# Kernel optimization log

Hardware: AMD Instinct MI355X
Metric: run time of the kernel (lower is better)

The kernel has to match this reference:

```python
import jax, jax.numpy as jnp
import numpy as np

N, E, IN, H, OUT = 50000, 600000, 256, 128, 40
EPS, GAMMA = 0.1, 0.1  # PyG AntiSymmetricConv defaults


def _build_norm(edge_index, n):
    # GCNConv normalization with added self loops: D^-1/2 (A+I) D^-1/2
    loops = jnp.arange(n, dtype=edge_index.dtype)
    src = jnp.concatenate([edge_index[0], loops])
    dst = jnp.concatenate([edge_index[1], loops])
    deg = jax.ops.segment_sum(jnp.ones(src.shape[0], dtype=jnp.float32), dst, num_segments=n)
    dinv = jnp.where(deg > 0, jax.lax.rsqrt(jnp.maximum(deg, 1e-12)), 0.0)
    return src, dst, dinv[src] * dinv[dst]


def _gcn(x, w, src, dst, norm, n):
    # GCNConv(bias=False): scatter normalized messages to target nodes
    m = (x @ w)[src] * norm[:, None]          # [E+N, d]
    return jax.ops.segment_sum(m, dst, num_segments=n)


def _antisym_conv(x, W, gcn_w, bias, src, dst, norm, num_iters):
    d = W.shape[0]
    aW = W - W.T - GAMMA * jnp.eye(d, dtype=W.dtype)  # antisymmetric weight
    n = x.shape[0]

    def step(h, _):
        upd = jnp.tanh(h @ aW.T + _gcn(h, gcn_w, src, dst, norm, n) + bias)
        return h + EPS * upd, None

    x, _ = jax.lax.scan(step, x, None, length=num_iters)
    return x


def setup_inputs() -> dict:
    key = jax.random.key(0)
    ks = jax.random.split(key, 16)
    s = lambda fan: 1.0 / np.sqrt(fan)
    return {
        "x": jax.random.normal(ks[0], (N, IN), dtype=jnp.float32),
        "edge_index": jax.random.randint(ks[1], (2, E), 0, N, dtype=jnp.int64),
        "w_hid": jax.random.normal(ks[2], (H, IN), dtype=jnp.float32) * s(IN),
        "b_hid": jax.random.normal(ks[3], (H,), dtype=jnp.float32) * s(IN),
        "W_a1": jax.random.normal(ks[4], (H, H), dtype=jnp.float32) * s(H),
        "gcn_w1": jax.random.normal(ks[5], (H, H), dtype=jnp.float32) * s(H),
        "b_a1": jax.random.normal(ks[6], (H,), dtype=jnp.float32) * s(H),
        "w_hid2": jax.random.normal(ks[7], (H // 2, H), dtype=jnp.float32) * s(H),
        "b_hid2": jax.random.normal(ks[8], (H // 2,), dtype=jnp.float32) * s(H),
        "W_a2": jax.random.normal(ks[9], (H // 2, H // 2), dtype=jnp.float32) * s(H // 2),
        "gcn_w2": jax.random.normal(ks[10], (H // 2, H // 2), dtype=jnp.float32) * s(H // 2),
        "b_a2": jax.random.normal(ks[11], (H // 2,), dtype=jnp.float32) * s(H // 2),
        "w_fc": jax.random.normal(ks[12], (OUT, H // 2), dtype=jnp.float32) * s(H // 2),
        "b_fc": jax.random.normal(ks[13], (OUT,), dtype=jnp.float32) * s(H // 2),
    }


def reference(x, edge_index, w_hid, b_hid, W_a1, gcn_w1, b_a1,
              w_hid2, b_hid2, W_a2, gcn_w2, b_a2, w_fc, b_fc):
    n = x.shape[0]
    src, dst, norm = _build_norm(edge_index, n)
    h = jax.nn.leaky_relu(x @ w_hid.T + b_hid)          # dropout is no-op in eval
    h = _antisym_conv(h, W_a1, gcn_w1, b_a1, src, dst, norm, num_iters=3)
    h = jax.nn.leaky_relu(h)
    h = jax.nn.leaky_relu(h @ w_hid2.T + b_hid2)
    h = _antisym_conv(h, W_a2, gcn_w2, b_a2, src, dst, norm, num_iters=1)
    out = h @ w_fc.T + b_fc
    return jax.nn.log_softmax(out, axis=1)
```

## Files before the change

kernel.cpp:

```cpp
#include <hip/hip_runtime.h>
#include <hip/hip_bf16.h>
#include <math.h>

typedef unsigned short u16;
typedef unsigned int   u32;
using short8  = __attribute__((ext_vector_type(8))) short;
using ushort8 = __attribute__((ext_vector_type(8))) unsigned short;
using f32x4   = __attribute__((ext_vector_type(4))) float;

static constexpr int NNODE = 50000;
static constexpr int NEDGE = 600000;
static constexpr float EPSC   = 0.1f;
static constexpr float GAMMAC = 0.1f;

static constexpr long long O_DINV   = 0;
static constexpr long long O_DEGI   = 50000;
static constexpr long long O_ROWPTR = 100000;
static constexpr long long O_CURSOR = 150004;
static constexpr long long O_GCUR   = 200052;
static constexpr long long O_ECSR   = 200260;
static constexpr long long O_WHB    = 1400260;
static constexpr long long O_G1TB   = O_WHB  + 16384;
static constexpr long long O_AW1B   = O_G1TB + 8192;
static constexpr long long O_W2B    = O_AW1B + 8192;
static constexpr long long O_AW2B   = O_W2B  + 4096;
static constexpr long long O_G2TB   = O_AW2B + 2048;
static constexpr long long O_WFCB   = O_G2TB + 2048;
static constexpr long long O_AGGB   = 3450004;
static constexpr long long O_HB0    = O_AGGB + 3200000;
static constexpr long long O_HB1    = O_HB0  + 3200000;
static constexpr long long O_S0     = O_HB1  + 3200000;
static constexpr long long O_S1     = O_S0   + 1600000;

__device__ __forceinline__ float bf2f(u16 u) {
    return __uint_as_float(((unsigned)u) << 16);
}
__device__ __forceinline__ u16 f2bf(float f) {
    unsigned u = __float_as_uint(f);
    return (u16)((u + 0x7FFFu + ((u >> 16) & 1u)) >> 16);
}
__device__ __forceinline__ float ftanh(float x) {
    float x2 = fminf(fmaxf(2.f * x, -30.f), 30.f);
    float e = __expf(x2);
    return (e - 1.f) * __builtin_amdgcn_rcpf(e + 1.f);
}
__device__ __forceinline__ u16 pk_fp8(float a, float b) {
    int pk = __builtin_amdgcn_cvt_pk_fp8_f32(a, b, 0, false);
    return (u16)(pk & 0xffff);
}
__device__ __forceinline__ void acc_fp8x4(float* a, u32 v, float w) {
    a[0] += __builtin_amdgcn_cvt_f32_fp8(v, 0) * w;
    a[1] += __builtin_amdgcn_cvt_f32_fp8(v, 1) * w;
    a[2] += __builtin_amdgcn_cvt_f32_fp8(v, 2) * w;
    a[3] += __builtin_amdgcn_cvt_f32_fp8(v, 3) * w;
}

__global__ __launch_bounds__(256) void prep_kernel(
    const float* __restrict__ w_hid, const float* __restrict__ W_a1,
    const float* __restrict__ gcn1,  const float* __restrict__ w2,
    const float* __restrict__ W_a2,  const float* __restrict__ gcn2,
    const float* __restrict__ wfc,   float* __restrict__ ws)
{
    int j = blockIdx.x * 256 + threadIdx.x;
    if (j < 32768) { ((u16*)(ws+O_WHB))[j] = f2bf(w_hid[j]); return; } j -= 32768;
    if (j < 16384) { int r=j>>7, c=j&127; ((u16*)(ws+O_G1TB))[j] = f2bf(gcn1[c*128+r]); return; } j -= 16384;
    if (j < 16384) { int r=j>>7, c=j&127;
                     ((u16*)(ws+O_AW1B))[j] = f2bf(W_a1[r*128+c] - W_a1[c*128+r] - (r==c?GAMMAC:0.f));
                     return; } j -= 16384;
    if (j < 8192)  { ((u16*)(ws+O_W2B))[j] = f2bf(w2[j]); return; } j -= 8192;
    if (j < 4096)  { int r=j>>6, c=j&63;
                     ((u16*)(ws+O_AW2B))[j] = f2bf(W_a2[r*64+c] - W_a2[c*64+r] - (r==c?GAMMAC:0.f));
                     return; } j -= 4096;
    if (j < 4096)  { int r=j>>6, c=j&63; ((u16*)(ws+O_G2TB))[j] = f2bf(gcn2[c*64+r]); return; } j -= 4096;
    if (j < 2560)  { ((u16*)(ws+O_WFCB))[j] = f2bf(wfc[j]); return; } j -= 2560;
    if (j < NNODE) { ((int*)(ws+O_DEGI))[j] = 0; return; } j -= NNODE;
    if (j == 0)    { ((int*)(ws+O_GCUR))[0] = 0; }
}

__global__ __launch_bounds__(256) void deg_count_kernel(const int* __restrict__ ei,
                                                        int* __restrict__ degi) {
    int e = blockIdx.x * 256 + threadIdx.x;
    if (e < NEDGE) atomicAdd(&degi[ei[NEDGE + e]], 1);
}
__global__ __launch_bounds__(256) void alloc_kernel(const int* __restrict__ degi,
                                                    float* __restrict__ dinv,
                                                    int* __restrict__ rowptr,
                                                    int* __restrict__ cursor,
                                                    int* __restrict__ gcur) {
    int i = blockIdx.x * 256 + threadIdx.x;
    if (i >= NNODE) return;
    int d = degi[i];
    dinv[i] = rsqrtf(1.0f + (float)d);
    int pos = atomicAdd(gcur, d);
    rowptr[i] = pos;
    cursor[i] = pos;
}
__global__ __launch_bounds__(256) void fill_kernel(const int* __restrict__ ei,
                                                   const float* __restrict__ dinv,
                                                   int* __restrict__ cursor,
                                                   int2* __restrict__ ecsr) {
    int e = blockIdx.x * 256 + threadIdx.x;
    if (e >= NEDGE) return;
    int s = ei[e], d = ei[NEDGE + e];
    int pos = atomicAdd(&cursor[d], 1);
    int2 v;
    v.x = s;
    v.y = __float_as_int(dinv[s] * dinv[d]);
    ecsr[pos] = v;
}

template<int KS, int NT, int AF32, int LOADACT, int EPI>
__global__ __launch_bounds__(256, 4) void mgemm(
    const void* __restrict__ Araw,
    const u16* __restrict__ Bt,
    const float* __restrict__ bias,
    float* __restrict__ outF,
    u16* __restrict__ outB,
    u16* __restrict__ outB8,
    int M, int Nn, int ldc)
{
    constexpr int K    = KS * 32;
    constexpr int KCHU = (K > 128) ? 128 : K;
    constexpr int KC   = KCHU / 32;
    constexpr int NCH  = K / KCHU;
    constexpr int P    = KCHU + 8;
    constexpr int ROWS = NT * 16;
    constexpr int CW   = NT * 16 + 1;
    constexpr int BSZ  = ROWS * P * 2;
    constexpr int ASZ  = 64 * CW * 4;
    constexpr int SMEM = BSZ > ASZ ? BSZ : ASZ;
    __shared__ __align__(16) char smem[SMEM];
    u16*   bl   = (u16*)smem;
    float* accL = (float*)smem;

    const int wave = threadIdx.x >> 6;
    const int lane = threadIdx.x & 63;
    const int m = lane & 15, q = lane >> 4;
    const int rowbase = blockIdx.x * 64 + wave * 16;
    const int row = rowbase + m;
    const bool rok = row < M;
    const short8 z8 = {0,0,0,0,0,0,0,0};

    short8 af[KS];
    if (AF32) {
        const float* apf = (const float*)Araw + (long long)row * K;
        #pragma unroll
        for (int k = 0; k < KS; ++k) {
            short8 t = z8;
            if (rok) {
                const float4* p = (const float4*)(apf + (k * 4 + q) * 8);
                float4 a = p[0], b = p[1];
                t[0]=(short)f2bf(a.x); t[1]=(short)f2bf(a.y); t[2]=(short)f2bf(a.z); t[3]=(short)f2bf(a.w);
                t[4]=(short)f2bf(b.x); t[5]=(short)f2bf(b.y); t[6]=(short)f2bf(b.z); t[7]=(short)f2bf(b.w);
            }
            af[k] = t;
        }
    } else {
        const short8* ap = (const short8*)((const u16*)Araw + (long long)row * K);
        #pragma unroll
        for (int k = 0; k < KS; ++k) af[k] = rok ? ap[k * 4 + q] : z8;
    }
    if (LOADACT) {
        #pragma unroll
        for (int k = 0; k < KS; ++k)
            #pragma unroll
            for (int e = 0; e < 8; ++e) {
                float f = bf2f((u16)af[k][e]);
                f = f > 0.f ? f : 0.01f * f;
                af[k][e] = (short)f2bf(f);
            }
    }

    f32x4 acc[NT];
    #pragma unroll
    for (int j = 0; j < NT; ++j) acc[j] = (f32x4){0.f,0.f,0.f,0.f};

    for (int ch = 0; ch < NCH; ++ch) {
        if (ch) __syncthreads();
        constexpr int CHUNKS = ROWS * (KCHU / 8);
        for (int t = threadIdx.x; t < CHUNKS; t += 256) {
            int r = t / (KCHU / 8), c = t - r * (KCHU / 8);
            short8 v = z8;
            if (r < Nn) v = *(const short8*)&Bt[(long long)r * K + ch * KCHU + c * 8];
            *(short8*)&bl[r * P + c * 8] = v;
        }
        __syncthreads();
        #pragma unroll
        for (int j = 0; j < NT; ++j) {
            #pragma unroll
            for (int k = 0; k < KC; ++k) {
                short8 bf_ = *(const short8*)&bl[(j * 16 + m) * P + k * 32 + q * 8];
                acc[j] = __builtin_amdgcn_mfma_f32_16x16x32_bf16(af[ch * KC + k], bf_, acc[j], 0, 0, 0);
            }
        }
    }

    __syncthreads();
    #pragma unroll
    for (int j = 0; j < NT; ++j)
        #pragma unroll
        for (int r = 0; r < 4; ++r)
            accL[(wave * 16 + q * 4 + r) * CW + j * 16 + m] = acc[j][r];
    __syncthreads();

    if (EPI == 3) {
        float mrow = 0.f, lrow = 0.f;
        if (lane < 16) {
            const float* rp = &accL[(wave * 16 + lane) * CW];
            float mx = -1e30f;
            for (int c = 0; c < Nn; ++c) mx = fmaxf(mx, rp[c] + bias[c]);
            float s = 0.f;
            for (int c = 0; c < Nn; ++c) s += expf(rp[c] + bias[c] - mx);
            mrow = mx; lrow = logf(s);
        }
        for (int rl = 0; rl < 16; ++rl) {
            float mm = __shfl(mrow, rl);
            float ll = __shfl(lrow, rl);
            int rowD = rowbase + rl;
            if (rowD < M && lane < Nn) {
                float v = accL[(wave * 16 + rl) * CW + lane] + bias[lane];
                outF[(long long)rowD * ldc + lane] = v - mm - ll;
            }
        }
        return;
    }

    const int c0 = lane * 2;
    if (c0 < NT * 16) {
        float2 bv = {0.f, 0.f};
        if (bias) {
            if (c0 < Nn)     bv.x = bias[c0];
            if (c0 + 1 < Nn) bv.y = bias[c0 + 1];
        }
        #pragma unroll
        for (int rl = 0; rl < 16; ++rl) {
            int rowD = rowbase + rl;
            if (rowD >= M) continue;
            float2 v = *(const float2*)&accL[(wave * 16 + rl) * CW + c0];
            long long o = (long long)rowD * ldc + c0;
            v.x += bv.x; v.y += bv.y;
            if (EPI == 1) {
                v.x = v.x > 0.f ? v.x : 0.01f * v.x;
                v.y = v.y > 0.f ? v.y : 0.01f * v.y;
            }
            if (c0 + 1 < Nn) {
                if (outB) { ushort2 ob; ob.x = f2bf(v.x); ob.y = f2bf(v.y);
                            *(ushort2*)&outB[o] = ob; }
                if (outB8) outB8[o >> 1] = pk_fp8(v.x, v.y);
                if (outF) { *(float2*)&outF[o] = v; }
            } else if (c0 < Nn) {
                if (outB) outB[o] = f2bf(v.x);
                if (outF) outF[o] = v.x;
            }
        }
    }
}

template<int KS, int NT>
__global__ __launch_bounds__(256, 4) void mgemm_conv(
    const u16* __restrict__ hA,
    const u16* __restrict__ gA,
    const u16* __restrict__ BtW,
    const u16* __restrict__ BtG,
    const float* __restrict__ bias,
    u16* __restrict__ outB,
    u16* __restrict__ outB8,
    int M)
{
    constexpr int K    = KS * 32;
    constexpr int Nn   = NT * 16;
    constexpr int P    = K + 8;
    constexpr int CW   = Nn + 1;
    constexpr int BSZ  = Nn * P * 2;
    constexpr int ASZ  = 64 * CW * 4;
    constexpr int SMEM = BSZ > ASZ ? BSZ : ASZ;
    __shared__ __align__(16) char smem[SMEM];
    u16*   bl   = (u16*)smem;
    float* accL = (float*)smem;

    const int wave = threadIdx.x >> 6;
    const int lane = threadIdx.x & 63;
    const int m = lane & 15, q = lane >> 4;
    const int rowbase = blockIdx.x * 64 + wave * 16;
    const int row = rowbase + m;
    const bool rok = row < M;
    const short8 z8 = {0,0,0,0,0,0,0,0};

    short8 af1[KS], af2[KS];
    {
        const short8* ap1 = (const short8*)(hA + (long long)row * K);
        const short8* ap2 = (const short8*)(gA + (long long)row * K);
        #pragma unroll
        for (int k = 0; k < KS; ++k) {
            af1[k] = rok ? ap1[k * 4 + q] : z8;
            af2[k] = rok ? ap2[k * 4 + q] : z8;
        }
    }

    f32x4 acc[NT];
    #pragma unroll
    for (int j = 0; j < NT; ++j) acc[j] = (f32x4){0.f,0.f,0.f,0.f};

    #pragma unroll
    for (int pass = 0; pass < 2; ++pass) {
        const u16* Bcur = pass ? BtG : BtW;
        if (pass) __syncthreads();
        constexpr int CHUNKS = Nn * (K / 8);
        for (int t = threadIdx.x; t < CHUNKS; t += 256) {
            int r = t / (K / 8), c = t - r * (K / 8);
            *(short8*)&bl[r * P + c * 8] = *(const short8*)&Bcur[(long long)r * K + c * 8];
        }
        __syncthreads();
        #pragma unroll
        for (int j = 0; j < NT; ++j) {
            #pragma unroll
            for (int k = 0; k < KS; ++k) {
                short8 bf_ = *(const short8*)&bl[(j * 16 + m) * P + k * 32 + q * 8];
                acc[j] = __builtin_amdgcn_mfma_f32_16x16x32_bf16(
                    pass ? af2[k] : af1[k], bf_, acc[j], 0, 0, 0);
            }
        }
    }

    __syncthreads();
    #pragma unroll
    for (int j = 0; j < NT; ++j)
        #pragma unroll
        for (int r = 0; r < 4; ++r)
            accL[(wave * 16 + q * 4 + r) * CW + j * 16 + m] = acc[j][r];
    __syncthreads();

    const int c0 = lane * 2;
    if (c0 < Nn) {
        float2 bv;
        bv.x = bias[c0]; bv.y = bias[c0 + 1];
        #pragma unroll
        for (int rl = 0; rl < 16; ++rl) {
            int rowD = rowbase + rl;
            if (rowD >= M) continue;
            float2 v = *(const float2*)&accL[(wave * 16 + rl) * CW + c0];
            long long o = (long long)rowD * Nn + c0;
            ushort2 hh = *(const ushort2*)&hA[o];
            float n0 = bf2f(hh.x) + EPSC * ftanh(v.x + bv.x);
            float n1 = bf2f(hh.y) + EPSC * ftanh(v.y + bv.y);
            ushort2 ob; ob.x = f2bf(n0); ob.y = f2bf(n1);
            *(ushort2*)&outB[o] = ob;
            if (outB8) outB8[o >> 1] = pk_fp8(n0, n1);
        }
    }
}

template<int HD>
__global__ __launch_bounds__(256) void gather_kernel(
    const int* __restrict__ rowptr, const int* __restrict__ degi,
    const int2* __restrict__ ecsr, const float* __restrict__ dinv,
    const u32* __restrict__ g8, u16* __restrict__ aggB)
{
    int node = (blockIdx.x * 256 + threadIdx.x) >> 6;
    int lane = threadIdx.x & 63;
    if (node >= NNODE) return;
    const int qr = lane >> 4, l4 = lane & 15;
    const int r0 = rowptr[node];
    const int r1 = r0 + degi[node];
    const float wself = dinv[node] * dinv[node];
    constexpr int EL = (HD == 128) ? 8 : 4;

    float a[EL];
    #pragma unroll
    for (int i = 0; i < EL; ++i) a[i] = 0.f;
    if (qr == 0) {
        if (HD == 128) {
            uint2 gv = ((const uint2*)g8)[(long long)node * 16 + l4];
            acc_fp8x4(a, gv.x, wself);
            acc_fp8x4(a + 4, gv.y, wself);
        } else {
            u32 gv = g8[(long long)node * 16 + l4];
            acc_fp8x4(a, gv, wself);
        }
    }

    for (int base = r0; base < r1; base += 64) {
        int idx = base + lane;
        int cs = 0; float cw = 0.f;
        if (idx < r1) { int2 ev = ecsr[idx]; cs = ev.x; cw = __int_as_float(ev.y); }
        int cnt = min(64, r1 - base);
        for (int j = 0; j < cnt; j += 4) {
            int jj = j + qr;
            int   s = __shfl(cs, jj);
            float w = __shfl(cw, jj);
            if (HD == 128) {
                uint2 gv = ((const uint2*)g8)[(long long)s * 16 + l4];
                acc_fp8x4(a, gv.x, w);
                acc_fp8x4(a + 4, gv.y, w);
            } else {
                u32 gv = g8[(long long)s * 16 + l4];
                acc_fp8x4(a, gv, w);
            }
        }
    }

    #pragma unroll
    for (int i = 0; i < EL; ++i) {
        a[i] += __shfl_xor(a[i], 16);
        a[i] += __shfl_xor(a[i], 32);
    }
    if (HD == 128) {
        float v0 = (qr == 0) ? a[0] : (qr == 1) ? a[2] : (qr == 2) ? a[4] : a[6];
        float v1 = (qr == 0) ? a[1] : (qr == 1) ? a[3] : (qr == 2) ? a[5] : a[7];
        long long o = (long long)node * 128 + l4 * 8 + qr * 2;
        ushort2 ob; ob.x = f2bf(v0); ob.y = f2bf(v1);
        *(ushort2*)&aggB[o] = ob;
    } else {
        float v = (qr == 0) ? a[0] : (qr == 1) ? a[1] : (qr == 2) ? a[2] : a[3];
        aggB[(long long)node * 64 + l4 * 4 + qr] = f2bf(v);
    }
}

extern "C" void kernel_launch(void* const* d_in, const int* in_sizes, int n_in,
                              void* d_out, int out_size, void* d_ws, size_t ws_size,
                              hipStream_t stream) {
    const float* x     = (const float*)d_in[0];
    const int*   ei    = (const int*)d_in[1];
    const float* w_hid = (const float*)d_in[2];
    const float* b_hid = (const float*)d_in[3];
    const float* W_a1  = (const float*)d_in[4];
    const float* gcn1  = (const float*)d_in[5];
    const float* b_a1  = (const float*)d_in[6];
    const float* w2    = (const float*)d_in[7];
    const float* b2    = (const float*)d_in[8];
    const float* W_a2  = (const float*)d_in[9];
    const float* gcn2  = (const float*)d_in[10];
    const float* b_a2  = (const float*)d_in[11];
    const float* wfc   = (const float*)d_in[12];
    const float* bfc   = (const float*)d_in[13];
    float* ws = (float*)d_ws;
    float* out = (float*)d_out;

    float* dinv   = ws + O_DINV;
    int*   degi   = (int*)(ws + O_DEGI);
    int*   rowptr = (int*)(ws + O_ROWPTR);
    int*   cursor = (int*)(ws + O_CURSOR);
    int*   gcur   = (int*)(ws + O_GCUR);
    int2*  ecsr   = (int2*)(ws + O_ECSR);
    u16* whB  = (u16*)(ws + O_WHB);
    u16* g1tB = (u16*)(ws + O_G1TB);
    u16* aw1B = (u16*)(ws + O_AW1B);
    u16* w2B  = (u16*)(ws + O_W2B);
    u16* aw2B = (u16*)(ws + O_AW2B);
    u16* g2tB = (u16*)(ws + O_G2TB);
    u16* wfcB = (u16*)(ws + O_WFCB);
    u16* aggB = (u16*)(ws + O_AGGB);
    u16* hB0  = (u16*)(ws + O_HB0);
    u16* hB1  = (u16*)(ws + O_HB1);
    u16* s0   = (u16*)(ws + O_S0);
    u16* s1   = (u16*)(ws + O_S1);

    const int nNodeB = (NNODE + 255) / 256;

    prep_kernel<<<(84480 + NNODE + 256 + 255) / 256, 256, 0, stream>>>(
        w_hid, W_a1, gcn1, w2, W_a2, gcn2, wfc, ws);
    deg_count_kernel<<<(NEDGE + 255) / 256, 256, 0, stream>>>(ei, degi);
    alloc_kernel<<<nNodeB, 256, 0, stream>>>(degi, dinv, rowptr, cursor, gcur);
    fill_kernel<<<(NEDGE + 255) / 256, 256, 0, stream>>>(ei, dinv, cursor, ecsr);

    const int gB = (NNODE + 63) / 64;
    const int gatherBlocks = (NNODE * 64 + 255) / 256;

    mgemm<8, 8, 1, 0, 1><<<gB, 256, 0, stream>>>(
        x, whB, b_hid, nullptr, hB0, s0, NNODE, 128, 128);

    u16* hBc = hB0; u16* hBo = hB1;
    u16* sC  = s0;  u16* sO  = s1;
    for (int it = 0; it < 3; ++it) {
        gather_kernel<128><<<gatherBlocks, 256, 0, stream>>>(
            rowptr, degi, ecsr, dinv, (const u32*)sC, aggB);
        mgemm_conv<4, 8><<<gB, 256, 0, stream>>>(
            hBc, aggB, aw1B, g1tB, b_a1, hBo, sO, NNODE);
        u16* tb = hBc; hBc = hBo; hBo = tb;
        u16* ts = sC;  sC = sO;  sO = ts;
    }

    mgemm<4, 4, 0, 1, 1><<<gB, 256, 0, stream>>>(
        hBc, w2B, b2, nullptr, hBo, sO, NNODE, 64, 64);
    u16* h2B = hBo; u16* s2 = sO;
    u16* spB = hBc;

    gather_kernel<64><<<gatherBlocks, 256, 0, stream>>>(
        rowptr, degi, ecsr, dinv, (const u32*)s2, aggB);
    mgemm_conv<2, 4><<<gB, 256, 0, stream>>>(
        h2B, aggB, aw2B, g2tB, b_a2, spB, nullptr, NNODE);

    mgemm<2, 3, 0, 0, 3><<<gB, 256, 0, stream>>>(
        spB, wfcB, bfc, out, nullptr, nullptr, NNODE, 40, 40);
}
```

Measured before the change: 398.3 us.

## Fuse neighbor gather into conv GEMM kernels and chain tail layers

The separate gather kernels are removed. Each conv kernel now gathers its 16 nodes per wave straight into LDS and feeds the aggregate to the MFMA pass. The last first-layer iteration also fuses the hidden2 linear plus leaky_relu, and the second conv fuses the final FC and log_softmax. This drops the aggB round-trip through global memory and several launches. In exchange, gather parallelism drops to one node at a time per wave, serialized inside the GEMM block, and LDS use and register pressure go up, which lowers occupancy (launch bounds 3).

Measured after the change: 519.1 us. 1.3x slower.

```diff
diff --git a/kernel.cpp b/kernel.cpp
--- a/kernel.cpp
+++ b/kernel.cpp
@@ -26,8 +26,7 @@
 static constexpr long long O_AW2B   = O_W2B  + 4096;
 static constexpr long long O_G2TB   = O_AW2B + 2048;
 static constexpr long long O_WFCB   = O_G2TB + 2048;
-static constexpr long long O_AGGB   = 3450004;
-static constexpr long long O_HB0    = O_AGGB + 3200000;
+static constexpr long long O_HB0    = 3450004;
 static constexpr long long O_HB1    = O_HB0  + 3200000;
 static constexpr long long O_S0     = O_HB1  + 3200000;
 static constexpr long long O_S1     = O_S0   + 1600000;
@@ -203,28 +202,6 @@
             accL[(wave * 16 + q * 4 + r) * CW + j * 16 + m] = acc[j][r];
     __syncthreads();
 
-    if (EPI == 3) {
-        float mrow = 0.f, lrow = 0.f;
-        if (lane < 16) {
-            const float* rp = &accL[(wave * 16 + lane) * CW];
-            float mx = -1e30f;
-            for (int c = 0; c < Nn; ++c) mx = fmaxf(mx, rp[c] + bias[c]);
-            float s = 0.f;
-            for (int c = 0; c < Nn; ++c) s += expf(rp[c] + bias[c] - mx);
-            mrow = mx; lrow = logf(s);
-        }
-        for (int rl = 0; rl < 16; ++rl) {
-            float mm = __shfl(mrow, rl);
-            float ll = __shfl(lrow, rl);
-            int rowD = rowbase + rl;
-            if (rowD < M && lane < Nn) {
-                float v = accL[(wave * 16 + rl) * CW + lane] + bias[lane];
-                outF[(long long)rowD * ldc + lane] = v - mm - ll;
-            }
-        }
-        return;
-    }
-
     const int c0 = lane * 2;
     if (c0 < NT * 16) {
         float2 bv = {0.f, 0.f};
@@ -256,27 +233,27 @@
     }
 }
 
-template<int KS, int NT>
-__global__ __launch_bounds__(256, 4) void mgemm_conv(
+template<int TAIL>
+__global__ __launch_bounds__(256, 3) void fconv1(
     const u16* __restrict__ hA,
-    const u16* __restrict__ gA,
-    const u16* __restrict__ BtW,
-    const u16* __restrict__ BtG,
+    const u32* __restrict__ g8,
+    const int* __restrict__ rowptr, const int* __restrict__ degi,
+    const int2* __restrict__ ecsr, const float* __restrict__ dinv,
+    const u16* __restrict__ BtW, const u16* __restrict__ BtG,
     const float* __restrict__ bias,
-    u16* __restrict__ outB,
-    u16* __restrict__ outB8,
+    u16* __restrict__ outB, u16* __restrict__ outB8,
+    const u16* __restrict__ w2W, const float* __restrict__ b2,
     int M)
 {
-    constexpr int K    = KS * 32;
-    constexpr int Nn   = NT * 16;
-    constexpr int P    = K + 8;
-    constexpr int CW   = Nn + 1;
-    constexpr int BSZ  = Nn * P * 2;
-    constexpr int ASZ  = 64 * CW * 4;
-    constexpr int SMEM = BSZ > ASZ ? BSZ : ASZ;
-    __shared__ __align__(16) char smem[SMEM];
+    constexpr int K  = 128, NT = 8, KS = 4;
+    constexpr int P  = K + 8;
+    constexpr int CW = NT * 16 + 1;
+    constexpr int BSZ = 128 * P * 2;
+    constexpr int R1  = BSZ;
+    __shared__ __align__(16) char smem[R1 + 64 * P * 2];
     u16*   bl   = (u16*)smem;
     float* accL = (float*)smem;
+    u16*   aggT = (u16*)(smem + R1);
 
     const int wave = threadIdx.x >> 6;
     const int lane = threadIdx.x & 63;
@@ -286,16 +263,56 @@
     const bool rok = row < M;
     const short8 z8 = {0,0,0,0,0,0,0,0};
 
-    short8 af1[KS], af2[KS];
-    {
-        const short8* ap1 = (const short8*)(hA + (long long)row * K);
-        const short8* ap2 = (const short8*)(gA + (long long)row * K);
-        #pragma unroll
-        for (int k = 0; k < KS; ++k) {
-            af1[k] = rok ? ap1[k * 4 + q] : z8;
-            af2[k] = rok ? ap2[k * 4 + q] : z8;
-        }
-    }
+    short8 af1[KS];
+    {
+        const short8* ap = (const short8*)(hA + (long long)row * K);
+        #pragma unroll
+        for (int k = 0; k < KS; ++k) af1[k] = rok ? ap[k * 4 + q] : z8;
+    }
+
+    {
+        const int qr = q, l4 = m;
+        for (int nn = 0; nn < 16; ++nn) {
+            int node = rowbase + nn;
+            if (node >= M) continue;
+            const int r0 = rowptr[node];
+            const int r1 = r0 + degi[node];
+            const float wself = dinv[node] * dinv[node];
+            float a[8] = {0.f,0.f,0.f,0.f,0.f,0.f,0.f,0.f};
+            if (qr == 0) {
+                uint2 gv = ((const uint2*)g8)[(long long)node * 16 + l4];
+                acc_fp8x4(a, gv.x, wself);
+                acc_fp8x4(a + 4, gv.y, wself);
+            }
+            for (int base = r0; base < r1; base += 64) {
+                int idx = base + lane;
+                int cs = 0; float cw = 0.f;
+                if (idx < r1) { int2 ev = ecsr[idx]; cs = ev.x; cw = __int_as_float(ev.y); }
+                int cnt = min(64, r1 - base);
+                for (int j = 0; j < cnt; j += 4) {
+                    int jj = j + qr;
+                    int   s = __shfl(cs, jj);
+                    float w = __shfl(cw, jj);
+                    uint2 gv = ((const uint2*)g8)[(long long)s * 16 + l4];
+                    acc_fp8x4(a, gv.x, w);
+                    acc_fp8x4(a + 4, gv.y, w);
+                }
+            }
+            #pragma unroll
+            for (int i = 0; i < 8; ++i) {
+                a[i] += __shfl_xor(a[i], 16);
+                a[i] += __shfl_xor(a[i], 32);
+            }
+            float v0 = (qr == 0) ? a[0] : (qr == 1) ? a[2] : (qr == 2) ? a[4] : a[6];
+            float v1 = (qr == 0) ? a[1] : (qr == 1) ? a[3] : (qr == 2) ? a[5] : a[7];
+            ushort2 ob; ob.x = f2bf(v0); ob.y = f2bf(v1);
+            *(ushort2*)&aggT[(wave * 16 + nn) * P + l4 * 8 + qr * 2] = ob;
+        }
+    }
+    short8 af2[KS];
+    #pragma unroll
+    for (int k = 0; k < KS; ++k)
+        af2[k] = *(const short8*)&aggT[(wave * 16 + m) * P + k * 32 + q * 8];
 
     f32x4 acc[NT];
     #pragma unroll
@@ -305,9 +322,9 @@
     for (int pass = 0; pass < 2; ++pass) {
         const u16* Bcur = pass ? BtG : BtW;
         if (pass) __syncthreads();
-        constexpr int CHUNKS = Nn * (K / 8);
+        constexpr int CHUNKS = 128 * (K / 8);
         for (int t = threadIdx.x; t < CHUNKS; t += 256) {
-            int r = t / (K / 8), c = t - r * (K / 8);
+            int r = t >> 4, c = t & 15;
             *(short8*)&bl[r * P + c * 8] = *(const short8*)&Bcur[(long long)r * K + c * 8];
         }
         __syncthreads();
@@ -331,88 +348,278 @@
     __syncthreads();
 
     const int c0 = lane * 2;
-    if (c0 < Nn) {
-        float2 bv;
-        bv.x = bias[c0]; bv.y = bias[c0 + 1];
+    if (TAIL == 0) {
+        float2 bv = {bias[c0], bias[c0 + 1]};
         #pragma unroll
         for (int rl = 0; rl < 16; ++rl) {
             int rowD = rowbase + rl;
             if (rowD >= M) continue;
             float2 v = *(const float2*)&accL[(wave * 16 + rl) * CW + c0];
-            long long o = (long long)rowD * Nn + c0;
+            long long o = (long long)rowD * K + c0;
             ushort2 hh = *(const ushort2*)&hA[o];
             float n0 = bf2f(hh.x) + EPSC * ftanh(v.x + bv.x);
             float n1 = bf2f(hh.y) + EPSC * ftanh(v.y + bv.y);
             ushort2 ob; ob.x = f2bf(n0); ob.y = f2bf(n1);
             *(ushort2*)&outB[o] = ob;
-            if (outB8) outB8[o >> 1] = pk_fp8(n0, n1);
-        }
-    }
-}
-
-template<int HD>
-__global__ __launch_bounds__(256) void gather_kernel(
+            outB8[o >> 1] = pk_fp8(n0, n1);
+        }
+        return;
+    }
+
+    {
+        float2 bv = {bias[c0], bias[c0 + 1]};
+        #pragma unroll
+        for (int rl = 0; rl < 16; ++rl) {
+            int rowD = rowbase + rl;
+            float n0 = 0.f, n1 = 0.f;
+            if (rowD < M) {
+                float2 v = *(const float2*)&accL[(wave * 16 + rl) * CW + c0];
+                long long o = (long long)rowD * K + c0;
+                ushort2 hh = *(const ushort2*)&hA[o];
+                n0 = bf2f(hh.x) + EPSC * ftanh(v.x + bv.x);
+                n1 = bf2f(hh.y) + EPSC * ftanh(v.y + bv.y);
+                n0 = n0 > 0.f ? n0 : 0.01f * n0;
+                n1 = n1 > 0.f ? n1 : 0.01f * n1;
+            }
+            ushort2 ob; ob.x = f2bf(n0); ob.y = f2bf(n1);
+            *(ushort2*)&aggT[(wave * 16 + rl) * P + c0] = ob;
+        }
+    }
+    __syncthreads();
+
+    short8 af3[KS];
+    #pragma unroll
+    for (int k = 0; k < KS; ++k)
+        af3[k] = *(const short8*)&aggT[(wave * 16 + m) * P + k * 32 + q * 8];
+
+    {
+        constexpr int CH2 = 64 * 16;
+        for (int t = threadIdx.x; t < CH2; t += 256) {
+            int r = t >> 4, c = t & 15;
+            *(short8*)&bl[r * P + c * 8] = *(const short8*)&w2W[(long long)r * K + c * 8];
+        }
+    }
+    __syncthreads();
+
+    f32x4 acc2[4];
+    #pragma unroll
+    for (int j = 0; j < 4; ++j) acc2[j] = (f32x4){0.f,0.f,0.f,0.f};
+    #pragma unroll
+    for (int j = 0; j < 4; ++j)
+        #pragma unroll
+        for (int k = 0; k < KS; ++k) {
+            short8 bf_ = *(const short8*)&bl[(j * 16 + m) * P + k * 32 + q * 8];
+            acc2[j] = __builtin_amdgcn_mfma_f32_16x16x32_bf16(af3[k], bf_, acc2[j], 0, 0, 0);
+        }
+
+    __syncthreads();
+    constexpr int CW2 = 65;
+    #pragma unroll
+    for (int j = 0; j < 4; ++j)
+        #pragma unroll
+        for (int r = 0; r < 4; ++r)
+            accL[(wave * 16 + q * 4 + r) * CW2 + j * 16 + m] = acc2[j][r];
+    __syncthreads();
+
+    if (c0 < 64) {
+        float2 bv = {b2[c0], b2[c0 + 1]};
+        #pragma unroll
+        for (int rl = 0; rl < 16; ++rl) {
+            int rowD = rowbase + rl;
+            if (rowD >= M) continue;
+            float2 v = *(const float2*)&accL[(wave * 16 + rl) * CW2 + c0];
+            v.x += bv.x; v.y += bv.y;
+            v.x = v.x > 0.f ? v.x : 0.01f * v.x;
+            v.y = v.y > 0.f ? v.y : 0.01f * v.y;
+            long long o = (long long)rowD * 64 + c0;
+            ushort2 ob; ob.x = f2bf(v.x); ob.y = f2bf(v.y);
+            *(ushort2*)&outB[o] = ob;
+            outB8[o >> 1] = pk_fp8(v.x, v.y);
+        }
+    }
+}
+
+__global__ __launch_bounds__(256, 4) void fconv2(
+    const u16* __restrict__ hA,
+    const u32* __restrict__ g8,
     const int* __restrict__ rowptr, const int* __restrict__ degi,
     const int2* __restrict__ ecsr, const float* __restrict__ dinv,
-    const u32* __restrict__ g8, u16* __restrict__ aggB)
+    const u16* __restrict__ BtW, const u16* __restrict__ BtG,
+    const float* __restrict__ bias,
+    const u16* __restrict__ wfcB, const float* __restrict__ bfc,
+    float* __restrict__ outF, int M)
 {
-    int node = (blockIdx.x * 256 + threadIdx.x) >> 6;
-    int lane = threadIdx.x & 63;
-    if (node >= NNODE) return;
-    const int qr = lane >> 4, l4 = lane & 15;
-    const int r0 = rowptr[node];
-    const int r1 = r0 + degi[node];
-    const float wself = dinv[node] * dinv[node];
-    constexpr int EL = (HD == 128) ? 8 : 4;
-
-    float a[EL];
-    #pragma unroll
-    for (int i = 0; i < EL; ++i) a[i] = 0.f;
-    if (qr == 0) {
-        if (HD == 128) {
-            uint2 gv = ((const uint2*)g8)[(long long)node * 16 + l4];
-            acc_fp8x4(a, gv.x, wself);
-            acc_fp8x4(a + 4, gv.y, wself);
-        } else {
-            u32 gv = g8[(long long)node * 16 + l4];
-            acc_fp8x4(a, gv, wself);
-        }
-    }
-
-    for (int base = r0; base < r1; base += 64) {
-        int idx = base + lane;
-        int cs = 0; float cw = 0.f;
-        if (idx < r1) { int2 ev = ecsr[idx]; cs = ev.x; cw = __int_as_float(ev.y); }
-        int cnt = min(64, r1 - base);
-        for (int j = 0; j < cnt; j += 4) {
-            int jj = j + qr;
-            int   s = __shfl(cs, jj);
-            float w = __shfl(cw, jj);
-            if (HD == 128) {
-                uint2 gv = ((const uint2*)g8)[(long long)s * 16 + l4];
-                acc_fp8x4(a, gv.x, w);
-                acc_fp8x4(a + 4, gv.y, w);
-            } else {
-                u32 gv = g8[(long long)s * 16 + l4];
-                acc_fp8x4(a, gv, w);
-            }
-        }
-    }
-
-    #pragma unroll
-    for (int i = 0; i < EL; ++i) {
-        a[i] += __shfl_xor(a[i], 16);
-        a[i] += __shfl_xor(a[i], 32);
-    }
-    if (HD == 128) {
-        float v0 = (qr == 0) ? a[0] : (qr == 1) ? a[2] : (qr == 2) ? a[4] : a[6];
-        float v1 = (qr == 0) ? a[1] : (qr == 1) ? a[3] : (qr == 2) ? a[5] : a[7];
-        long long o = (long long)node * 128 + l4 * 8 + qr * 2;
-        ushort2 ob; ob.x = f2bf(v0); ob.y = f2bf(v1);
-        *(ushort2*)&aggB[o] = ob;
-    } else {
-        float v = (qr == 0) ? a[0] : (qr == 1) ? a[1] : (qr == 2) ? a[2] : a[3];
-        aggB[(long long)node * 64 + l4 * 4 + qr] = f2bf(v);
+    constexpr int K  = 64, NT = 4, KS = 2;
+    constexpr int P  = K + 8;
+    constexpr int CW = 65;
+    constexpr int R1 = 64 * CW * 4;
+    __shared__ __align__(16) char smem[R1 + 64 * P * 2];
+    u16*   bl   = (u16*)smem;
+    float* accL = (float*)smem;
+    u16*   aggT = (u16*)(smem + R1);
+
+    const int wave = threadIdx.x >> 6;
+    const int lane = threadIdx.x & 63;
+    const int m = lane & 15, q = lane >> 4;
+    const int rowbase = blockIdx.x * 64 + wave * 16;
+    const int row = rowbase + m;
+    const bool rok = row < M;
+    const short8 z8 = {0,0,0,0,0,0,0,0};
+
+    short8 af1[KS];
+    {
+        const short8* ap = (const short8*)(hA + (long long)row * K);
+        #pragma unroll
+        for (int k = 0; k < KS; ++k) af1[k] = rok ? ap[k * 4 + q] : z8;
+    }
+
+    {
+        const int qr = q, l4 = m;
+        for (int nn = 0; nn < 16; ++nn) {
+            int node = rowbase + nn;
+            if (node >= M) continue;
+            const int r0 = rowptr[node];
+            const int r1 = r0 + degi[node];
+            const float wself = dinv[node] * dinv[node];
+            float a[4] = {0.f,0.f,0.f,0.f};
+            if (qr == 0) {
+                u32 gv = g8[(long long)node * 16 + l4];
+                acc_fp8x4(a, gv, wself);
+            }
+            for (int base = r0; base < r1; base += 64) {
+                int idx = base + lane;
+                int cs = 0; float cw = 0.f;
+                if (idx < r1) { int2 ev = ecsr[idx]; cs = ev.x; cw = __int_as_float(ev.y); }
+                int cnt = min(64, r1 - base);
+                for (int j = 0; j < cnt; j += 4) {
+                    int jj = j + qr;
+                    int   s = __shfl(cs, jj);
+                    float w = __shfl(cw, jj);
+                    u32 gv = g8[(long long)s * 16 + l4];
+                    acc_fp8x4(a, gv, w);
+                }
+            }
+            #pragma unroll
+            for (int i = 0; i < 4; ++i) {
+                a[i] += __shfl_xor(a[i], 16);
+                a[i] += __shfl_xor(a[i], 32);
+            }
+            float v = (qr == 0) ? a[0] : (qr == 1) ? a[1] : (qr == 2) ? a[2] : a[3];
+            aggT[(wave * 16 + nn) * P + l4 * 4 + qr] = f2bf(v);
+        }
+    }
+    short8 af2[KS];
+    #pragma unroll
+    for (int k = 0; k < KS; ++k)
+        af2[k] = *(const short8*)&aggT[(wave * 16 + m) * P + k * 32 + q * 8];
+
+    f32x4 acc[NT];
+    #pragma unroll
+    for (int j = 0; j < NT; ++j) acc[j] = (f32x4){0.f,0.f,0.f,0.f};
+
+    #pragma unroll
+    for (int pass = 0; pass < 2; ++pass) {
+        const u16* Bcur = pass ? BtG : BtW;
+        if (pass) __syncthreads();
+        constexpr int CHUNKS = 64 * (K / 8);
+        for (int t = threadIdx.x; t < CHUNKS; t += 256) {
+            int r = t >> 3, c = t & 7;
+            *(short8*)&bl[r * P + c * 8] = *(const short8*)&Bcur[(long long)r * K + c * 8];
+        }
+        __syncthreads();
+        #pragma unroll
+        for (int j = 0; j < NT; ++j)
+            #pragma unroll
+            for (int k = 0; k < KS; ++k) {
+                short8 bf_ = *(const short8*)&bl[(j * 16 + m) * P + k * 32 + q * 8];
+                acc[j] = __builtin_amdgcn_mfma_f32_16x16x32_bf16(
+                    pass ? af2[k] : af1[k], bf_, acc[j], 0, 0, 0);
+            }
+    }
+
+    __syncthreads();
+    #pragma unroll
+    for (int j = 0; j < NT; ++j)
+        #pragma unroll
+        for (int r = 0; r < 4; ++r)
+            accL[(wave * 16 + q * 4 + r) * CW + j * 16 + m] = acc[j][r];
+    __syncthreads();
+
+    {
+        const int c0 = lane * 2;
+        float2 bv = {bias[c0 & 63], bias[(c0 + 1) & 63]};
+        if (c0 < 64) {
+            #pragma unroll
+            for (int rl = 0; rl < 16; ++rl) {
+                int rowD = rowbase + rl;
+                float n0 = 0.f, n1 = 0.f;
+                if (rowD < M) {
+                    float2 v = *(const float2*)&accL[(wave * 16 + rl) * CW + c0];
+                    long long o = (long long)rowD * 64 + c0;
+                    ushort2 hh = *(const ushort2*)&hA[o];
+                    n0 = bf2f(hh.x) + EPSC * ftanh(v.x + bv.x);
+                    n1 = bf2f(hh.y) + EPSC * ftanh(v.y + bv.y);
+                }
+                ushort2 ob; ob.x = f2bf(n0); ob.y = f2bf(n1);
+                *(ushort2*)&aggT[(wave * 16 + rl) * P + c0] = ob;
+            }
+        }
+    }
+    __syncthreads();
+
+    short8 af4[KS];
+    #pragma unroll
+    for (int k = 0; k < KS; ++k)
+        af4[k] = *(const short8*)&aggT[(wave * 16 + m) * P + k * 32 + q * 8];
+
+    {
+        constexpr int CHF = 48 * 8;
+        for (int t = threadIdx.x; t < CHF; t += 256) {
+            int r = t >> 3, c = t & 7;
+            short8 v = z8;
+            if (r < 40) v = *(const short8*)&wfcB[(long long)r * K + c * 8];
+            *(short8*)&bl[r * P + c * 8] = v;
+        }
+    }
+    __syncthreads();
+
+    f32x4 acc3[3];
+    #pragma unroll
+    for (int j = 0; j < 3; ++j) acc3[j] = (f32x4){0.f,0.f,0.f,0.f};
+    #pragma unroll
+    for (int j = 0; j < 3; ++j)
+        #pragma unroll
+        for (int k = 0; k < KS; ++k) {
+            short8 bf_ = *(const short8*)&bl[(j * 16 + m) * P + k * 32 + q * 8];
+            acc3[j] = __builtin_amdgcn_mfma_f32_16x16x32_bf16(af4[k], bf_, acc3[j], 0, 0, 0);
+        }
+
+    __syncthreads();
+    constexpr int CW3 = 49;
+    #pragma unroll
+    for (int j = 0; j < 3; ++j)
+        #pragma unroll
+        for (int r = 0; r < 4; ++r)
+            accL[(wave * 16 + q * 4 + r) * CW3 + j * 16 + m] = acc3[j][r];
+    __syncthreads();
+
+    float mrow = 0.f, lrow = 0.f;
+    if (lane < 16) {
+        const float* rp = &accL[(wave * 16 + lane) * CW3];
+        float mx = -1e30f;
+        for (int c = 0; c < 40; ++c) mx = fmaxf(mx, rp[c] + bfc[c]);
+        float s = 0.f;
+        for (int c = 0; c < 40; ++c) s += expf(rp[c] + bfc[c] - mx);
+        mrow = mx; lrow = logf(s);
+    }
+    for (int rl = 0; rl < 16; ++rl) {
+        float mm = __shfl(mrow, rl);
+        float ll = __shfl(lrow, rl);
+        int rowD = rowbase + rl;
+        if (rowD < M && lane < 40) {
+            float v = accL[(wave * 16 + rl) * CW3 + lane] + bfc[lane];
+            outF[(long long)rowD * 40 + lane] = v - mm - ll;
+        }
     }
 }
 
@@ -449,7 +656,6 @@
     u16* aw2B = (u16*)(ws + O_AW2B);
     u16* g2tB = (u16*)(ws + O_G2TB);
     u16* wfcB = (u16*)(ws + O_WFCB);
-    u16* aggB = (u16*)(ws + O_AGGB);
     u16* hB0  = (u16*)(ws + O_HB0);
     u16* hB1  = (u16*)(ws + O_HB1);
     u16* s0   = (u16*)(ws + O_S0);
@@ -464,32 +670,17 @@
     fill_kernel<<<(NEDGE + 255) / 256, 256, 0, stream>>>(ei, dinv, cursor, ecsr);
 
     const int gB = (NNODE + 63) / 64;
-    const int gatherBlocks = (NNODE * 64 + 255) / 256;
 
     mgemm<8, 8, 1, 0, 1><<<gB, 256, 0, stream>>>(
         x, whB, b_hid, nullptr, hB0, s0, NNODE, 128, 128);
 
-    u16* hBc = hB0; u16* hBo = hB1;
-    u16* sC  = s0;  u16* sO  = s1;
-    for (int it = 0; it < 3; ++it) {
-        gather_kernel<128><<<gatherBlocks, 256, 0, stream>>>(
-            rowptr, degi, ecsr, dinv, (const u32*)sC, aggB);
-        mgemm_conv<4, 8><<<gB, 256, 0, stream>>>(
-            hBc, aggB, aw1B, g1tB, b_a1, hBo, sO, NNODE);
-        u16* tb = hBc; hBc = hBo; hBo = tb;
-        u16* ts = sC;  sC = sO;  sO = ts;
-    }
-
-    mgemm<4, 4, 0, 1, 1><<<gB, 256, 0, stream>>>(
-        hBc, w2B, b2, nullptr, hBo, sO, NNODE, 64, 64);
-    u16* h2B = hBo; u16* s2 = sO;
-    u16* spB = hBc;
-
-    gather_kernel<64><<<gatherBlocks, 256, 0, stream>>>(
-        rowptr, degi, ecsr, dinv, (const u32*)s2, aggB);
-    mgemm_conv<2, 4><<<gB, 256, 0, stream>>>(
-        h2B, aggB, aw2B, g2tB, b_a2, spB, nullptr, NNODE);
-
-    mgemm<2, 3, 0, 0, 3><<<gB, 256, 0, stream>>>(
-        spB, wfcB, bfc, out, nullptr, nullptr, NNODE, 40, 40);
-}
+    fconv1<0><<<gB, 256, 0, stream>>>(hB0, (const u32*)s0, rowptr, degi, ecsr, dinv,
+                                      aw1B, g1tB, b_a1, hB1, s1, nullptr, nullptr, NNODE);
+    fconv1<0><<<gB, 256, 0, stream>>>(hB1, (const u32*)s1, rowptr, degi, ecsr, dinv,
+                                      aw1B, g1tB, b_a1, hB0, s0, nullptr, nullptr, NNODE);
+    fconv1<1><<<gB, 256, 0, stream>>>(hB0, (const u32*)s0, rowptr, degi, ecsr, dinv,
+                                      aw1B, g1tB, b_a1, hB1, s1, w2B, b2, NNODE);
+
+    fconv2<<<gB, 256, 0, stream>>>(hB1, (const u32*)s1, rowptr, degi, ecsr, dinv,
+                                   aw2B, g2tB, b_a2, wfcB, bfc, out, NNODE);
+}
```
